# Optimization experiments

Measured on AMD Instinct MI355X. Metric: run time of the kernel, lower is better.

The kernel has to match this reference:

```python
import jax, jax.numpy as jnp
import numpy as np

F_, OF, OW, L, H, NH = 40, 8, 24, 3, 128, 4
G = F_ // OF  # 5 groups
B, T = 32, 512


def setup_inputs() -> dict:
    key = jax.random.key(0)
    ks = jax.random.split(key, 17)
    s = 0.08
    rn = lambda k, shape: jax.random.normal(k, shape, jnp.float32) * s
    return {
        "x": jax.random.normal(ks[0], (B, F_, T), jnp.float32),
        # per-feature stacked 3-layer LSTM params (PyTorch gate order i,f,g,o)
        "w_ih0": rn(ks[1], (F_, 4 * H, 1)),
        "w_ih12": rn(ks[2], (L - 1, F_, 4 * H, H)),
        "w_hh": rn(ks[3], (L, F_, 4 * H, H)),
        "b_ih": rn(ks[4], (L, F_, 4 * H)),
        "b_hh": rn(ks[5], (L, F_, 4 * H)),
        # per-group MHA params
        "g_wqkv": rn(ks[6], (G, 3 * H, H)),
        "g_bqkv": rn(ks[7], (G, 3 * H)),
        "g_wo": rn(ks[8], (G, H, H)),
        "g_bo": rn(ks[9], (G, H)),
        # final MHA params
        "f_wqkv": rn(ks[10], (3 * H, H)),
        "f_bqkv": rn(ks[11], (3 * H,)),
        "f_wo": rn(ks[12], (H, H)),
        "f_bo": rn(ks[13], (H,)),
        # output FC
        "fc_w": rn(ks[14], (OF * OW, H)),
        "fc_b": rn(ks[15], (OF * OW,)),
    }


def _lstm_layer(xw, whh, bhh):
    # xw: [F,B,T,4H] precomputed input projections; scan over time
    h0 = jnp.zeros(xw.shape[:2] + (H,), xw.dtype)
    def step(carry, xt):
        h, c = carry
        gates = xt + jnp.einsum('fbh,fgh->fbg', h, whh) + bhh[:, None, :]
        i, f, g, o = jnp.split(gates, 4, axis=-1)
        c = jax.nn.sigmoid(f) * c + jax.nn.sigmoid(i) * jnp.tanh(g)
        h = jax.nn.sigmoid(o) * jnp.tanh(c)
        return (h, c), h
    (hT, _), hs = jax.lax.scan(step, (h0, h0), jnp.moveaxis(xw, 2, 0))
    return jnp.moveaxis(hs, 0, 2), hT  # seq [F,B,T,H], last [F,B,H]


def _mha(q, k, v, wqkv, bqkv, wo, bo):
    wq, wk, wv = jnp.split(wqkv, 3, axis=0)
    bq, bk, bv = jnp.split(bqkv, 3, axis=0)
    hd = H // NH
    def proj(t, w, b):
        p = t @ w.T + b
        return p.reshape(t.shape[:-1] + (NH, hd)).swapaxes(-3, -2)  # [..,NH,S,hd]
    qh, kh, vh = proj(q, wq, bq), proj(k, wk, bk), proj(v, wv, bv)
    scores = jnp.einsum('bnqd,bnkd->bnqk', qh, kh) / np.float32(np.sqrt(hd))
    attn = jax.nn.softmax(scores, axis=-1)
    out = jnp.einsum('bnqk,bnkd->bnqd', attn, vh).swapaxes(-3, -2).reshape(q.shape)
    return out @ wo.T + bo


def reference(x, w_ih0, w_ih12, w_hh, b_ih, b_hh, g_wqkv, g_bqkv, g_wo, g_bo,
              f_wqkv, f_bqkv, f_wo, f_bo, fc_w, fc_b):
    bsz = x.shape[0]
    h_seq = jnp.transpose(x, (1, 0, 2))[..., None]  # [F,B,T,1]
    h_last = None
    for l in range(L):  # 3 stacked LSTM layers, all 40 feature-LSTMs batched
        wih = w_ih0 if l == 0 else w_ih12[l - 1]
        xw = jnp.einsum('fbti,fgi->fbtg', h_seq, wih) + b_ih[l][:, None, None, :]
        h_seq, h_last = _lstm_layer(xw, w_hh[l], b_hh[l])
    features = jnp.transpose(h_last, (1, 0, 2))  # [B,F,H]
    groups = features.reshape(bsz, G, OF, H).swapaxes(0, 1)  # [G,B,OF,H]
    gattn = jax.vmap(lambda g, w, b, wo, bo: _mha(g, g, g, w, b, wo, bo))(
        groups, g_wqkv, g_bqkv, g_wo, g_bo)  # [G,B,OF,H]
    pooled = gattn.mean(axis=2).swapaxes(0, 1)  # [B,G,H]
    fin = _mha(pooled, pooled, pooled, f_wqkv, f_bqkv, f_wo, f_bo)  # [B,G,H]
    emb = fin[:, 0, :]  # target_coin_index = 0
    return (emb @ fc_w.T + fc_b).reshape(bsz, OF, OW)
```

## Files before the change

### kernel.cpp

```cpp
#include <hip/hip_runtime.h>
#include <cstdint>
#include <cstddef>


#define NFEAT 40
#define TDIM  512

typedef __bf16 bf16x8 __attribute__((ext_vector_type(8)));
typedef float floatx4 __attribute__((ext_vector_type(4)));
typedef int   intx4   __attribute__((ext_vector_type(4)));
typedef unsigned short u16;
typedef unsigned long long u64;

#if __has_builtin(__builtin_amdgcn_exp2f)
#define EXP2F __builtin_amdgcn_exp2f
#else
#define EXP2F exp2f
#endif
#if __has_builtin(__builtin_amdgcn_rcpf)
#define RCPF __builtin_amdgcn_rcpf
#else
#define RCPF(x) (1.f / (x))
#endif

#define MF(a, b, c) __builtin_amdgcn_mfma_f32_16x16x32_bf16( \
    __builtin_bit_cast(bf16x8, (a)), __builtin_bit_cast(bf16x8, (b)), (c), 0, 0, 0)

__device__ __forceinline__ float bf2f(u16 s) {
  union { unsigned u; float f; } v; v.u = ((unsigned)s) << 16; return v.f;
}
__device__ __forceinline__ unsigned f2bf(float f) {
  union { float f; unsigned u; } v; v.f = f;
  unsigned u = v.u + 0x7fffu + ((v.u >> 16) & 1u);
  return (u >> 16);
}

#define RING_FSTRIDE 1048576
#define RING_TSTRIDE 4096
#define RING_MASK    255

__global__ void prep_kernel(const float* __restrict__ w_ih12,
                            const float* __restrict__ w_hh,
                            const float* __restrict__ b_ih,
                            const float* __restrict__ b_hh,
                            u16* __restrict__ Whh,
                            u16* __restrict__ Wih,
                            float* __restrict__ biasAll,
                            int* __restrict__ flags)
{
  const int N_hh = 3 * NFEAT * 512 * 128;
  const int N_ih = 2 * NFEAT * 512 * 128;
  const int NB   = 3 * NFEAT * 512;
  const int NF   = 192;
  const int total = N_hh + N_ih + NB + NF;
  for (int idx = blockIdx.x * blockDim.x + threadIdx.x; idx < total;
       idx += gridDim.x * blockDim.x) {
    if (idx < N_hh) {
      Whh[idx] = (u16)f2bf(w_hh[idx]);
    } else if (idx < N_hh + N_ih) {
      int i = idx - N_hh;
      Wih[i] = (u16)f2bf(w_ih12[i]);
    } else if (idx < N_hh + N_ih + NB) {
      int i = idx - N_hh - N_ih;
      biasAll[i] = b_ih[i] + b_hh[i];
    } else {
      flags[idx - N_hh - N_ih - NB] = 0;
    }
  }
}

template <int LAYER>
__device__ __forceinline__ void lstm_body(
    const u16* __restrict__ Wh, const u16* __restrict__ Wx,
    const float* __restrict__ bias,
    const float* __restrict__ xin, const float* __restrict__ w0,
    const u16* __restrict__ ringIn, u16* __restrict__ ringOut,
    u16* __restrict__ hlast,
    int* __restrict__ flagIn, int* __restrict__ flagOut,
    int f, int half, u16* __restrict__ Abase)
{
  constexpr bool IS_L0   = (LAYER == 0);
  constexpr bool IS_LAST = (LAYER == 2);

  const int tid  = threadIdx.x;
  const int wave = tid >> 6;
  const int lane = tid & 63;
  const int m15  = lane & 15;
  const int q    = lane >> 4;
  const int kb   = q * 8;
  const int wq4  = wave * 16 + q * 4;

#define ALDS(P, M, K) (Abase + ((P) * 16 + (M)) * 136 + (K))

  intx4 whf[4][4];
  const size_t wbase = (size_t)f * 512 * 128;
#pragma unroll
  for (int g = 0; g < 4; ++g)
#pragma unroll
    for (int kt = 0; kt < 4; ++kt)
      whf[g][kt] = *(const intx4*)(Wh + wbase +
          (size_t)(g * 128 + wave * 16 + m15) * 128 + kt * 32 + kb);

  intx4 wxf[4][4];
  if constexpr (!IS_L0) {
#pragma unroll
    for (int g = 0; g < 4; ++g)
#pragma unroll
      for (int kt = 0; kt < 4; ++kt)
        wxf[g][kt] = *(const intx4*)(Wx + wbase +
            (size_t)(g * 128 + wave * 16 + m15) * 128 + kt * 32 + kb);
  }

  floatx4 bv[4], w0v[4];
#pragma unroll
  for (int g = 0; g < 4; ++g) {
    bv[g] = *(const floatx4*)(bias + f * 512 + g * 128 + wq4);
    if constexpr (IS_L0) w0v[g] = *(const floatx4*)(w0 + f * 512 + g * 128 + wq4);
  }

  for (int idx = tid; idx < 2 * 16 * 136; idx += 512) Abase[idx] = 0;

  if constexpr (LAYER >= 1) {
    if (tid == 0) {
      while (__hip_atomic_load(flagIn, __ATOMIC_RELAXED,
                               __HIP_MEMORY_SCOPE_AGENT) < 11)
        __builtin_amdgcn_s_sleep(2);
      __threadfence();
    }
  }
  __syncthreads();

  const u16* xbase = (LAYER >= 1)
      ? ringIn + (size_t)f * RING_FSTRIDE + (half * 16 + m15) * 128 + kb
      : nullptr;
  const float* xsbase = IS_L0
      ? xin + ((size_t)(half * 16 + m15) * NFEAT + f) * 512
      : nullptr;

  floatx4 accx0[4], accx1[4];
  intx4 xf0[4], xf1[4];
  float xsc[2] = {0.f, 0.f};

  if constexpr (!IS_L0) {
    intx4 p0[4];
#pragma unroll
    for (int kt = 0; kt < 4; ++kt) p0[kt]  = *(const intx4*)(xbase + kt * 32);
#pragma unroll
    for (int kt = 0; kt < 4; ++kt)
      xf0[kt] = *(const intx4*)(xbase + 1 * RING_TSTRIDE + kt * 32);
#pragma unroll
    for (int kt = 0; kt < 4; ++kt)
      xf1[kt] = *(const intx4*)(xbase + 2 * RING_TSTRIDE + kt * 32);
#pragma unroll
    for (int g = 0; g < 4; ++g) {
      floatx4 a = bv[g];
#pragma unroll
      for (int kt = 0; kt < 4; ++kt) a = MF(wxf[g][kt], p0[kt], a);
      accx0[g] = a;
    }
  } else {
    const float x0 = xsbase[0];
    xsc[0] = xsbase[1];
    xsc[1] = xsbase[2];
#pragma unroll
    for (int g = 0; g < 4; ++g) accx0[g] = bv[g] + w0v[g] * x0;
  }

  float creg[4] = {0.f, 0.f, 0.f, 0.f};
  u16* hb_ring = (LAYER <= 1)
      ? ringOut + (size_t)f * RING_FSTRIDE + (half * 16 + m15) * 128 + wq4
      : nullptr;
  u64 hdef64 = 0;

#define LSTM_STEP(PC, ACC_C, ACC_N, XF_C, T)                                   \
  {                                                                            \
                                             \
    if (((T) & 7) == 0 && (T) > 0) {                                           \
      if (tid == 0) {                                                          \
        if constexpr (LAYER <= 1)                                              \
          __hip_atomic_store(flagOut, (T) - 1, __ATOMIC_RELAXED,               \
                             __HIP_MEMORY_SCOPE_AGENT);                        \
        if constexpr (LAYER >= 1) {                                            \
          int tgt = (T) + 11; if (tgt > 512) tgt = 512;                        \
          while (__hip_atomic_load(flagIn, __ATOMIC_RELAXED,                   \
                                   __HIP_MEMORY_SCOPE_AGENT) < tgt)            \
            __builtin_amdgcn_s_sleep(2);                                       \
        }                                                                      \
        __threadfence();                                                       \
      }                                                                        \
      if constexpr (LAYER >= 1) __syncthreads();                               \
    }                                                                          \
                              \
    if constexpr (!IS_LAST) {                                                  \
      if ((T) > 0)                                                             \
        __hip_atomic_store(                                                    \
            (u64*)(hb_ring + (size_t)(((T) - 1) & RING_MASK) * RING_TSTRIDE),  \
            hdef64, __ATOMIC_RELAXED, __HIP_MEMORY_SCOPE_AGENT);               \
    }                                                                          \
                                            \
    intx4 xn0, xn1, xn2, xn3;                                                  \
    float xns = 0.f;                                                           \
    {                                                                          \
      const int tl = ((T) + 3 < TDIM) ? (T) + 3 : TDIM - 1;                    \
      if constexpr (!IS_L0) {                                                  \
        const u16* xp = xbase + (size_t)(tl & RING_MASK) * RING_TSTRIDE;       \
        xn0 = *(const intx4*)(xp);                                             \
        xn1 = *(const intx4*)(xp + 32);                                        \
        xn2 = *(const intx4*)(xp + 64);                                        \
        xn3 = *(const intx4*)(xp + 96);                                        \
      } else {                                                                 \
        xns = xsbase[tl];                                                      \
      }                                                                        \
    }                                                                          \
                                                     \
    intx4 hf0 = *(const intx4*)ALDS(PC, m15, kb);                              \
    intx4 hf1 = *(const intx4*)ALDS(PC, m15, 32 + kb);                         \
    intx4 hf2 = *(const intx4*)ALDS(PC, m15, 64 + kb);                         \
    intx4 hf3 = *(const intx4*)ALDS(PC, m15, 96 + kb);                         \
                                                   \
    floatx4 ac0 = MF(whf[0][0], hf0, ACC_C[0]);                                \
    floatx4 ac1 = MF(whf[1][0], hf0, ACC_C[1]);                                \
    floatx4 ac2 = MF(whf[2][0], hf0, ACC_C[2]);                                \
    floatx4 ac3 = MF(whf[3][0], hf0, ACC_C[3]);                                \
    ac0 = MF(whf[0][1], hf1, ac0); ac1 = MF(whf[1][1], hf1, ac1);              \
    ac2 = MF(whf[2][1], hf1, ac2); ac3 = MF(whf[3][1], hf1, ac3);              \
    ac0 = MF(whf[0][2], hf2, ac0); ac1 = MF(whf[1][2], hf2, ac1);              \
    ac2 = MF(whf[2][2], hf2, ac2); ac3 = MF(whf[3][2], hf2, ac3);              \
    ac0 = MF(whf[0][3], hf3, ac0); ac1 = MF(whf[1][3], hf3, ac1);              \
    ac2 = MF(whf[2][3], hf3, ac2); ac3 = MF(whf[3][3], hf3, ac3);              \
             \
    if constexpr (!IS_L0) {                                                    \
      floatx4 n0 = bv[0], n1 = bv[1], n2 = bv[2], n3 = bv[3];                  \
      n0 = MF(wxf[0][0], XF_C[0], n0); n1 = MF(wxf[1][0], XF_C[0], n1);        \
      n2 = MF(wxf[2][0], XF_C[0], n2); n3 = MF(wxf[3][0], XF_C[0], n3);        \
      n0 = MF(wxf[0][1], XF_C[1], n0); n1 = MF(wxf[1][1], XF_C[1], n1);        \
      n2 = MF(wxf[2][1], XF_C[1], n2); n3 = MF(wxf[3][1], XF_C[1], n3);        \
      n0 = MF(wxf[0][2], XF_C[2], n0); n1 = MF(wxf[1][2], XF_C[2], n1);        \
      n2 = MF(wxf[2][2], XF_C[2], n2); n3 = MF(wxf[3][2], XF_C[2], n3);        \
      n0 = MF(wxf[0][3], XF_C[3], n0); n1 = MF(wxf[1][3], XF_C[3], n1);        \
      n2 = MF(wxf[2][3], XF_C[3], n2); n3 = MF(wxf[3][3], XF_C[3], n3);        \
      ACC_N[0] = n0; ACC_N[1] = n1; ACC_N[2] = n2; ACC_N[3] = n3;              \
      XF_C[0] = xn0; XF_C[1] = xn1; XF_C[2] = xn2; XF_C[3] = xn3;              \
    } else {                                                                   \
      const float xn = xsc[PC];                                                \
      ACC_N[0] = bv[0] + w0v[0] * xn; ACC_N[1] = bv[1] + w0v[1] * xn;          \
      ACC_N[2] = bv[2] + w0v[2] * xn; ACC_N[3] = bv[3] + w0v[3] * xn;          \
      xsc[PC] = xns;                                                           \
    }                                                                          \
                             \
    unsigned hlo, hhi;                                                         \
    {                                                                          \
      float hv[4];                                                             \
      _Pragma("unroll")                                                        \
      for (int r = 0; r < 4; ++r) {                                            \
        const float gi = ac0[r], gf = ac1[r], gg = ac2[r], go = ac3[r];        \
        const float si = RCPF(1.f + EXP2F(-1.44269504f * gi));                 \
        const float sf = RCPF(1.f + EXP2F(-1.44269504f * gf));                 \
        const float so = RCPF(1.f + EXP2F(-1.44269504f * go));                 \
        const float tg = 2.f * RCPF(1.f + EXP2F(-2.88539008f * gg)) - 1.f;     \
        const float c  = sf * creg[r] + si * tg;                               \
        creg[r] = c;                                                           \
        const float th = 2.f * RCPF(1.f + EXP2F(-2.88539008f * c)) - 1.f;      \
        hv[r] = so * th;                                                       \
      }                                                                        \
      hlo = (f2bf(hv[1]) << 16) | f2bf(hv[0]);                                 \
      hhi = (f2bf(hv[3]) << 16) | f2bf(hv[2]);                                 \
    }                                                                          \
    uint2 hp; hp.x = hlo; hp.y = hhi;                                          \
    *(uint2*)ALDS((PC) ^ 1, m15, wq4) = hp;                                    \
    hdef64 = ((u64)hhi << 32) | (u64)hlo;                                      \
    __syncthreads();                                                           \
  }

#pragma unroll 1
  for (int t = 0; t < TDIM; t += 2) {
    LSTM_STEP(0, accx0, accx1, xf0, t);
    LSTM_STEP(1, accx1, accx0, xf1, t + 1);
  }
#undef LSTM_STEP
#undef ALDS

  if constexpr (!IS_LAST) {
    __hip_atomic_store((u64*)(hb_ring + (size_t)255 * RING_TSTRIDE), hdef64,
                       __ATOMIC_RELAXED, __HIP_MEMORY_SCOPE_AGENT);
    __syncthreads();
    if (tid == 0) {
      __threadfence();
      __hip_atomic_store(flagOut, 512, __ATOMIC_RELAXED,
                         __HIP_MEMORY_SCOPE_AGENT);
    }
  } else {
    uint2 hp;
    hp.x = (unsigned)(hdef64 & 0xffffffffull);
    hp.y = (unsigned)(hdef64 >> 32);
    *(uint2*)(hlast + ((size_t)f * 32 + half * 16 + m15) * 128 + wq4) = hp;
  }
}

__global__ __launch_bounds__(512, 2) void lstm_fused(
    const u16* __restrict__ Whh, const u16* __restrict__ Wih,
    const float* __restrict__ biasAll,
    const float* __restrict__ xin, const float* __restrict__ w0,
    u16* __restrict__ ring0, u16* __restrict__ ring1,
    u16* __restrict__ hlast, int* __restrict__ flags)
{
  __shared__ __align__(16) u16 A[2 * 16 * 136];
  const int layer = blockIdx.x / 80;
  const int bx    = blockIdx.x % 80;
  const int f = bx >> 1, half = bx & 1;
  const size_t LSL = (size_t)NFEAT * 512 * 128;

  if (layer == 0) {
    lstm_body<0>(Whh, nullptr, biasAll, xin, w0,
                 nullptr, ring0, nullptr,
                 nullptr, flags + bx, f, half, A);
  } else if (layer == 1) {
    lstm_body<1>(Whh + LSL, Wih, biasAll + NFEAT * 512, nullptr, nullptr,
                 ring0, ring1, nullptr,
                 flags + bx, flags + 80 + bx, f, half, A);
  } else {
    lstm_body<2>(Whh + 2 * LSL, Wih + LSL, biasAll + 2 * NFEAT * 512,
                 nullptr, nullptr, ring1, nullptr, hlast,
                 flags + 80 + bx, nullptr, f, half, A);
  }
}

__global__ void gattn_kernel(const u16* __restrict__ hlast,
                             const float* __restrict__ g_wqkv,
                             const float* __restrict__ g_bqkv,
                             const float* __restrict__ g_wo,
                             const float* __restrict__ g_bo,
                             float* __restrict__ pooled)
{
  const int tid = threadIdx.x;
  const int g = blockIdx.x >> 5;
  const int b = blockIdx.x & 31;

  __shared__ float feat[8][128];
  __shared__ float qkv[8][384];
  __shared__ float sc[4][8][8];
  __shared__ float colsum[4][8];
  __shared__ float poolin[128];

  for (int idx = tid; idx < 8 * 128; idx += 128) {
    int of = idx >> 7, j = idx & 127;
    int f = g * 8 + of;
    feat[of][j] = bf2f(hlast[((size_t)f * 32 + b) * 128 + j]);
  }
  __syncthreads();
  for (int idx = tid; idx < 8 * 384; idx += 128) {
    int of = idx / 384, r = idx - of * 384;
    const float* wr = g_wqkv + ((size_t)g * 384 + r) * 128;
    float s = 0.f;
    for (int j = 0; j < 128; ++j) s += feat[of][j] * wr[j];
    qkv[of][r] = s + g_bqkv[g * 384 + r];
  }
  __syncthreads();
  for (int idx = tid; idx < 256; idx += 128) {
    int n = idx >> 6, qp = (idx >> 3) & 7, kp = idx & 7;
    float s = 0.f;
    for (int d = 0; d < 32; ++d)
      s += qkv[qp][n * 32 + d] * qkv[kp][128 + n * 32 + d];
    sc[n][qp][kp] = s * 0.17677669529663687f;
  }
  __syncthreads();
  if (tid < 32) {
    int n = tid >> 3, qp = tid & 7;
    float mx = -1e30f;
    for (int kp = 0; kp < 8; ++kp) mx = fmaxf(mx, sc[n][qp][kp]);
    float e[8], sum = 0.f;
    for (int kp = 0; kp < 8; ++kp) { e[kp] = __expf(sc[n][qp][kp] - mx); sum += e[kp]; }
    float inv = 1.f / sum;
    for (int kp = 0; kp < 8; ++kp) sc[n][qp][kp] = e[kp] * inv;
  }
  __syncthreads();
  if (tid < 32) {
    int n = tid >> 3, kp = tid & 7;
    float s = 0.f;
    for (int qp = 0; qp < 8; ++qp) s += sc[n][qp][kp];
    colsum[n][kp] = s;
  }
  __syncthreads();
  {
    int n = tid >> 5;
    float s = 0.f;
    for (int kp = 0; kp < 8; ++kp) s += colsum[n][kp] * qkv[kp][256 + tid];
    poolin[tid] = s;
  }
  __syncthreads();
  {
    const float* wr = g_wo + ((size_t)g * 128 + tid) * 128;
    float s = 0.f;
    for (int i = 0; i < 128; ++i) s += poolin[i] * wr[i];
    pooled[((size_t)b * 5 + g) * 128 + tid] = s * 0.125f + g_bo[g * 128 + tid];
  }
}

__global__ void final_kernel(const float* __restrict__ pooled,
                             const float* __restrict__ f_wqkv,
                             const float* __restrict__ f_bqkv,
                             const float* __restrict__ f_wo,
                             const float* __restrict__ f_bo,
                             const float* __restrict__ fc_w,
                             const float* __restrict__ fc_b,
                             float* __restrict__ out)
{
  const int tid = threadIdx.x;
  const int b = blockIdx.x;

  __shared__ float P[5][128];
  __shared__ float q0[128];
  __shared__ float kbuf[5][128];
  __shared__ float vbuf[5][128];
  __shared__ float attn[4][5];
  __shared__ float ao[128];
  __shared__ float fin[128];

  for (int idx = tid; idx < 640; idx += 192) {
    int g = idx >> 7, j = idx & 127;
    P[g][j] = pooled[((size_t)b * 5 + g) * 128 + j];
  }
  __syncthreads();
  for (int idx = tid; idx < 1408; idx += 192) {
    int kind, pos, r;
    if (idx < 128)       { kind = 0; pos = 0;                 r = idx; }
    else if (idx < 768)  { kind = 1; pos = (idx - 128) >> 7;  r = (idx - 128) & 127; }
    else                 { kind = 2; pos = (idx - 768) >> 7;  r = (idx - 768) & 127; }
    const int wrow = kind * 128 + r;
    const float* wr = f_wqkv + (size_t)wrow * 128;
    const float* src = P[kind == 0 ? 0 : pos];
    float s = 0.f;
    for (int j = 0; j < 128; ++j) s += src[j] * wr[j];
    s += f_bqkv[wrow];
    if (kind == 0) q0[r] = s;
    else if (kind == 1) kbuf[pos][r] = s;
    else vbuf[pos][r] = s;
  }
  __syncthreads();
  if (tid < 20) {
    int n = tid / 5, kp = tid - n * 5;
    float s = 0.f;
    for (int d = 0; d < 32; ++d) s += q0[n * 32 + d] * kbuf[kp][n * 32 + d];
    attn[n][kp] = s * 0.17677669529663687f;
  }
  __syncthreads();
  if (tid < 4) {
    float mx = -1e30f;
    for (int kp = 0; kp < 5; ++kp) mx = fmaxf(mx, attn[tid][kp]);
    float sum = 0.f;
    for (int kp = 0; kp < 5; ++kp) { float e = __expf(attn[tid][kp] - mx); attn[tid][kp] = e; sum += e; }
    float inv = 1.f / sum;
    for (int kp = 0; kp < 5; ++kp) attn[tid][kp] *= inv;
  }
  __syncthreads();
  if (tid < 128) {
    int n = tid >> 5;
    float s = 0.f;
    for (int kp = 0; kp < 5; ++kp) s += attn[n][kp] * vbuf[kp][tid];
    ao[tid] = s;
  }
  __syncthreads();
  if (tid < 128) {
    const float* wr = f_wo + (size_t)tid * 128;
    float s = 0.f;
    for (int i = 0; i < 128; ++i) s += ao[i] * wr[i];
    fin[tid] = s + f_bo[tid];
  }
  __syncthreads();
  {
    const float* wr = fc_w + (size_t)tid * 128;
    float s = 0.f;
    for (int j = 0; j < 128; ++j) s += fin[j] * wr[j];
    out[(size_t)b * 192 + tid] = s + fc_b[tid];
  }
}

extern "C" void kernel_launch(void* const* d_in, const int* in_sizes, int n_in,
                              void* d_out, int out_size, void* d_ws, size_t ws_size,
                              hipStream_t stream)
{
  const float* x      = (const float*)d_in[0];
  const float* w_ih0  = (const float*)d_in[1];
  const float* w_ih12 = (const float*)d_in[2];
  const float* w_hh   = (const float*)d_in[3];
  const float* b_ih   = (const float*)d_in[4];
  const float* b_hh   = (const float*)d_in[5];
  const float* g_wqkv = (const float*)d_in[6];
  const float* g_bqkv = (const float*)d_in[7];
  const float* g_wo   = (const float*)d_in[8];
  const float* g_bo   = (const float*)d_in[9];
  const float* f_wqkv = (const float*)d_in[10];
  const float* f_bqkv = (const float*)d_in[11];
  const float* f_wo   = (const float*)d_in[12];
  const float* f_bo   = (const float*)d_in[13];
  const float* fc_w   = (const float*)d_in[14];
  const float* fc_b   = (const float*)d_in[15];

  const size_t N_hh = (size_t)3 * NFEAT * 512 * 128;
  const size_t N_ih = (size_t)2 * NFEAT * 512 * 128;
  const size_t NB   = (size_t)3 * NFEAT * 512;
  const size_t RSZ  = (size_t)NFEAT * 256 * 4096;

  u16* Whh       = (u16*)d_ws;
  u16* Wih       = Whh + N_hh;
  float* biasAll = (float*)(Wih + N_ih);
  u16* ring0     = (u16*)(biasAll + NB);
  u16* ring1     = ring0 + RSZ;
  u16* hlast     = ring1 + RSZ;
  int* flags     = (int*)(hlast + (size_t)NFEAT * 32 * 128);
  float* pooled  = (float*)(flags + 192);

  prep_kernel<<<2048, 256, 0, stream>>>(w_ih12, w_hh, b_ih, b_hh,
                                        Whh, Wih, biasAll, flags);

  lstm_fused<<<240, 512, 0, stream>>>(Whh, Wih, biasAll, x, w_ih0,
                                      ring0, ring1, hlast, flags);

  gattn_kernel<<<160, 128, 0, stream>>>(hlast, g_wqkv, g_bqkv, g_wo, g_bo, pooled);
  final_kernel<<<32, 192, 0, stream>>>(pooled, f_wqkv, f_bqkv, f_wo, f_bo,
                                       fc_w, fc_b, (float*)d_out);
}
```

Baseline: 1.058 ms.

## Fold -log2e into weights, fuse LSTM gate math, relax cross-layer sync

Pre-scales all LSTM weights and biases by -log2(e) during bf16 conversion, so gate pre-activations feed exp2 directly. The sigmoid/tanh chain is rewritten algebraically to use fewer reciprocals per cell. The prep kernel is vectorised to float4. Cross-layer flag synchronisation moves from every 8 steps to every 16 with a larger lag, adds a consumer-progress flag as ring backpressure, and replaces atomic ring stores with plain stores. The intent is to cut transcendental and reciprocal work and synchronisation stalls on the serial recurrence, at some risk to numerical accuracy and memory-ordering correctness.

```diff
diff --git a/kernel.cpp b/kernel.cpp
--- a/kernel.cpp
+++ b/kernel.cpp
@@ -8,9 +8,9 @@
 
 typedef __bf16 bf16x8 __attribute__((ext_vector_type(8)));
 typedef float floatx4 __attribute__((ext_vector_type(4)));
+typedef float floatx2 __attribute__((ext_vector_type(2)));
 typedef int   intx4   __attribute__((ext_vector_type(4)));
 typedef unsigned short u16;
-typedef unsigned long long u64;
 
 #if __has_builtin(__builtin_amdgcn_exp2f)
 #define EXP2F __builtin_amdgcn_exp2f
@@ -26,6 +26,8 @@
 #define MF(a, b, c) __builtin_amdgcn_mfma_f32_16x16x32_bf16( \
     __builtin_bit_cast(bf16x8, (a)), __builtin_bit_cast(bf16x8, (b)), (c), 0, 0, 0)
 
+#define NEG_LOG2E -1.44269504f
+
 __device__ __forceinline__ float bf2f(u16 s) {
   union { unsigned u; float f; } v; v.u = ((unsigned)s) << 16; return v.f;
 }
@@ -48,23 +50,26 @@
                             float* __restrict__ biasAll,
                             int* __restrict__ flags)
 {
-  const int N_hh = 3 * NFEAT * 512 * 128;
-  const int N_ih = 2 * NFEAT * 512 * 128;
-  const int NB   = 3 * NFEAT * 512;
-  const int NF   = 192;
-  const int total = N_hh + N_ih + NB + NF;
+  const int N_hh4 = 3 * NFEAT * 512 * 128 / 4;
+  const int N_ih4 = 2 * NFEAT * 512 * 128 / 4;
+  const int NB    = 3 * NFEAT * 512;
+  const int NF    = 384;
+  const int total = N_hh4 + N_ih4 + NB + NF;
   for (int idx = blockIdx.x * blockDim.x + threadIdx.x; idx < total;
        idx += gridDim.x * blockDim.x) {
-    if (idx < N_hh) {
-      Whh[idx] = (u16)f2bf(w_hh[idx]);
-    } else if (idx < N_hh + N_ih) {
-      int i = idx - N_hh;
-      Wih[i] = (u16)f2bf(w_ih12[i]);
-    } else if (idx < N_hh + N_ih + NB) {
-      int i = idx - N_hh - N_ih;
-      biasAll[i] = b_ih[i] + b_hh[i];
+    if (idx < N_hh4 + N_ih4) {
+      const bool ih = (idx >= N_hh4);
+      const int i4 = (ih ? idx - N_hh4 : idx) * 4;
+      const float4 v = *(const float4*)((ih ? w_ih12 : w_hh) + i4);
+      uint2 p;
+      p.x = (f2bf(v.y * NEG_LOG2E) << 16) | f2bf(v.x * NEG_LOG2E);
+      p.y = (f2bf(v.w * NEG_LOG2E) << 16) | f2bf(v.z * NEG_LOG2E);
+      *(uint2*)((ih ? Wih : Whh) + i4) = p;
+    } else if (idx < N_hh4 + N_ih4 + NB) {
+      int i = idx - N_hh4 - N_ih4;
+      biasAll[i] = (b_ih[i] + b_hh[i]) * NEG_LOG2E;
     } else {
-      flags[idx - N_hh - N_ih - NB] = 0;
+      flags[idx - N_hh4 - N_ih4 - NB] = 0;
     }
   }
 }
@@ -76,7 +81,10 @@
     const float* __restrict__ xin, const float* __restrict__ w0,
     const u16* __restrict__ ringIn, u16* __restrict__ ringOut,
     u16* __restrict__ hlast,
-    int* __restrict__ flagIn, int* __restrict__ flagOut,
+    int* __restrict__ flagIn,
+    int* __restrict__ flagOut,
+    int* __restrict__ flagConsIn,
+    int* __restrict__ flagConsOut,
     int f, int half, u16* __restrict__ Abase)
 {
   constexpr bool IS_L0   = (LAYER == 0);
@@ -115,7 +123,10 @@
 #pragma unroll
   for (int g = 0; g < 4; ++g) {
     bv[g] = *(const floatx4*)(bias + f * 512 + g * 128 + wq4);
-    if constexpr (IS_L0) w0v[g] = *(const floatx4*)(w0 + f * 512 + g * 128 + wq4);
+    if constexpr (IS_L0) {
+      floatx4 wv = *(const floatx4*)(w0 + f * 512 + g * 128 + wq4);
+      w0v[g] = wv * NEG_LOG2E;
+    }
   }
 
   for (int idx = tid; idx < 2 * 16 * 136; idx += 512) Abase[idx] = 0;
@@ -123,7 +134,7 @@
   if constexpr (LAYER >= 1) {
     if (tid == 0) {
       while (__hip_atomic_load(flagIn, __ATOMIC_RELAXED,
-                               __HIP_MEMORY_SCOPE_AGENT) < 11)
+                               __HIP_MEMORY_SCOPE_AGENT) < 19)
         __builtin_amdgcn_s_sleep(2);
       __threadfence();
     }
@@ -170,32 +181,40 @@
   u16* hb_ring = (LAYER <= 1)
       ? ringOut + (size_t)f * RING_FSTRIDE + (half * 16 + m15) * 128 + wq4
       : nullptr;
-  u64 hdef64 = 0;
+  uint2 hdef;
 
 #define LSTM_STEP(PC, ACC_C, ACC_N, XF_C, T)                                   \
   {                                                                            \
-                                             \
-    if (((T) & 7) == 0 && (T) > 0) {                                           \
+                                            \
+    if (((T) & 15) == 0 && (T) > 0) {                                          \
       if (tid == 0) {                                                          \
-        if constexpr (LAYER <= 1)                                              \
-          __hip_atomic_store(flagOut, (T) - 1, __ATOMIC_RELAXED,               \
-                             __HIP_MEMORY_SCOPE_AGENT);                        \
         if constexpr (LAYER >= 1) {                                            \
-          int tgt = (T) + 11; if (tgt > 512) tgt = 512;                        \
+          int tgt = (T) + 19; if (tgt > 512) tgt = 512;                        \
           while (__hip_atomic_load(flagIn, __ATOMIC_RELAXED,                   \
                                    __HIP_MEMORY_SCOPE_AGENT) < tgt)            \
             __builtin_amdgcn_s_sleep(2);                                       \
         }                                                                      \
-        __threadfence();                                                       \
+        if constexpr (LAYER <= 1) {                                            \
+                               \
+          while (__hip_atomic_load(flagConsIn, __ATOMIC_RELAXED,               \
+                                   __HIP_MEMORY_SCOPE_AGENT) < (T) - 290)      \
+            __builtin_amdgcn_s_sleep(2);                                       \
+        }                                                                      \
+        __threadfence();       \
+        if constexpr (LAYER <= 1)                                              \
+          __hip_atomic_store(flagOut, (T) - 2, __ATOMIC_RELAXED,               \
+                             __HIP_MEMORY_SCOPE_AGENT);                        \
+        if constexpr (LAYER >= 1)                                              \
+          __hip_atomic_store(flagConsOut, (T), __ATOMIC_RELAXED,               \
+                             __HIP_MEMORY_SCOPE_AGENT);                        \
       }                                                                        \
       if constexpr (LAYER >= 1) __syncthreads();                               \
     }                                                                          \
-                              \
+                                 \
     if constexpr (!IS_LAST) {                                                  \
       if ((T) > 0)                                                             \
-        __hip_atomic_store(                                                    \
-            (u64*)(hb_ring + (size_t)(((T) - 1) & RING_MASK) * RING_TSTRIDE),  \
-            hdef64, __ATOMIC_RELAXED, __HIP_MEMORY_SCOPE_AGENT);               \
+        *(uint2*)(hb_ring + (size_t)(((T) - 1) & RING_MASK) * RING_TSTRIDE) =  \
+            hdef;                                                              \
     }                                                                          \
                                             \
     intx4 xn0, xn1, xn2, xn3;                                                  \
@@ -247,28 +266,29 @@
       ACC_N[2] = bv[2] + w0v[2] * xn; ACC_N[3] = bv[3] + w0v[3] * xn;          \
       xsc[PC] = xns;                                                           \
     }                                                                          \
-                             \
+                 \
     unsigned hlo, hhi;                                                         \
     {                                                                          \
       float hv[4];                                                             \
       _Pragma("unroll")                                                        \
       for (int r = 0; r < 4; ++r) {                                            \
-        const float gi = ac0[r], gf = ac1[r], gg = ac2[r], go = ac3[r];        \
-        const float si = RCPF(1.f + EXP2F(-1.44269504f * gi));                 \
-        const float sf = RCPF(1.f + EXP2F(-1.44269504f * gf));                 \
-        const float so = RCPF(1.f + EXP2F(-1.44269504f * go));                 \
-        const float tg = 2.f * RCPF(1.f + EXP2F(-2.88539008f * gg)) - 1.f;     \
-        const float c  = sf * creg[r] + si * tg;                               \
+        const float Ei = EXP2F(ac0[r]);                                        \
+        const float Ef = EXP2F(ac1[r]);                                        \
+        const float Eg = EXP2F(2.f * ac2[r]);                                  \
+        const float Eo = EXP2F(ac3[r]);                                        \
+        const float Pp = (1.f + Ei) * (1.f + Eg);                              \
+        const float Qq = 1.f + Ef;                                             \
+        const float c  = (creg[r] * Pp + Qq * (1.f - Eg)) * RCPF(Qq * Pp);     \
         creg[r] = c;                                                           \
-        const float th = 2.f * RCPF(1.f + EXP2F(-2.88539008f * c)) - 1.f;      \
-        hv[r] = so * th;                                                       \
+        const float Ec = EXP2F(-2.88539008f * c);                              \
+        hv[r] = (1.f - Ec) * RCPF((1.f + Ec) * (1.f + Eo));                    \
       }                                                                        \
       hlo = (f2bf(hv[1]) << 16) | f2bf(hv[0]);                                 \
       hhi = (f2bf(hv[3]) << 16) | f2bf(hv[2]);                                 \
     }                                                                          \
     uint2 hp; hp.x = hlo; hp.y = hhi;                                          \
     *(uint2*)ALDS((PC) ^ 1, m15, wq4) = hp;                                    \
-    hdef64 = ((u64)hhi << 32) | (u64)hlo;                                      \
+    hdef = hp;                                                                 \
     __syncthreads();                                                           \
   }
 
@@ -281,8 +301,7 @@
 #undef ALDS
 
   if constexpr (!IS_LAST) {
-    __hip_atomic_store((u64*)(hb_ring + (size_t)255 * RING_TSTRIDE), hdef64,
-                       __ATOMIC_RELAXED, __HIP_MEMORY_SCOPE_AGENT);
+    *(uint2*)(hb_ring + (size_t)(511 & RING_MASK) * RING_TSTRIDE) = hdef;
     __syncthreads();
     if (tid == 0) {
       __threadfence();
@@ -290,10 +309,7 @@
                          __HIP_MEMORY_SCOPE_AGENT);
     }
   } else {
-    uint2 hp;
-    hp.x = (unsigned)(hdef64 & 0xffffffffull);
-    hp.y = (unsigned)(hdef64 >> 32);
-    *(uint2*)(hlast + ((size_t)f * 32 + half * 16 + m15) * 128 + wq4) = hp;
+    *(uint2*)(hlast + ((size_t)f * 32 + half * 16 + m15) * 128 + wq4) = hdef;
   }
 }
 
@@ -313,15 +329,18 @@
   if (layer == 0) {
     lstm_body<0>(Whh, nullptr, biasAll, xin, w0,
                  nullptr, ring0, nullptr,
-                 nullptr, flags + bx, f, half, A);
+                 nullptr, flags + bx, flags + 160 + bx, nullptr,
+                 f, half, A);
   } else if (layer == 1) {
     lstm_body<1>(Whh + LSL, Wih, biasAll + NFEAT * 512, nullptr, nullptr,
                  ring0, ring1, nullptr,
-                 flags + bx, flags + 80 + bx, f, half, A);
+                 flags + bx, flags + 80 + bx, flags + 240 + bx,
+                 flags + 160 + bx, f, half, A);
   } else {
     lstm_body<2>(Whh + 2 * LSL, Wih + LSL, biasAll + 2 * NFEAT * 512,
                  nullptr, nullptr, ring1, nullptr, hlast,
-                 flags + 80 + bx, nullptr, f, half, A);
+                 flags + 80 + bx, nullptr, nullptr, flags + 240 + bx,
+                 f, half, A);
   }
 }
 
@@ -508,9 +527,9 @@
   u16* ring1     = ring0 + RSZ;
   u16* hlast     = ring1 + RSZ;
   int* flags     = (int*)(hlast + (size_t)NFEAT * 32 * 128);
-  float* pooled  = (float*)(flags + 192);
-
-  prep_kernel<<<2048, 256, 0, stream>>>(w_ih12, w_hh, b_ih, b_hh,
+  float* pooled  = (float*)(flags + 384);
+
+  prep_kernel<<<4096, 256, 0, stream>>>(w_ih12, w_hh, b_ih, b_hh,
                                         Whh, Wih, biasAll, flags);
 
   lstm_fused<<<240, 512, 0, stream>>>(Whh, Wih, biasAll, x, w_ih0,
```

Result: faster. 977.8 us (-7.6%).
